# Kernel tuning notes

Hardware: AMD Instinct MI355X
Metric: run time of the kernel (lower is better)

Reference implementation:

```python
import jax, jax.numpy as jnp
import numpy as np

B, NPG, K_DYN, H, C = 8, 4096, 8, 2, 64   # graphs, nodes/graph, kNN, heads, head dim
N = B * NPG
E = 524288
CAP = 20.0
NEG = 0.2


def _leaky(x):
    return jax.nn.leaky_relu(x, NEG)


def _bn(x, g, b):
    # BatchNorm1d, training-mode statistics over the node dim (biased var, eps=1e-5)
    m = jnp.mean(x, 0)
    v = jnp.mean((x - m) ** 2, 0)
    return (x - m) * jax.lax.rsqrt(v + 1e-5) * g + b


def _gatv2(x, src, dst, wl, bl, wr, br, att, bias, ea=None, we=None):
    # PyG GATv2Conv, heads=H, concat=False (mean over heads), dropout in eval mode
    n = x.shape[0]
    xl = (x @ wl + bl).reshape(n, H, C)   # source transform
    xr = (x @ wr + br).reshape(n, H, C)   # target transform
    e = xl[src] + xr[dst]                 # [E,H,C]
    if ea is not None:
        e = e + (ea @ we).reshape(-1, H, C)
    e = _leaky(e)
    logit = jnp.sum(e * att, -1)          # [E,H]
    m = jax.ops.segment_max(logit, dst, num_segments=n)
    m = jnp.where(jnp.isfinite(m), m, 0.0)
    ex = jnp.exp(logit - m[dst])
    den = jax.ops.segment_sum(ex, dst, num_segments=n) + 1e-16
    alpha = ex / den[dst]                 # segment softmax over incoming edges
    out = jax.ops.segment_sum(alpha[..., None] * xl[src], dst, num_segments=n)
    return jnp.mean(out, 1) + bias        # concat=False -> mean over heads


def _dyn_agg(h, w1, b1, w2, b2):
    # dynamic kNN in feature space (per graph, detached), gather-MLP-mean aggregation
    h3 = h.reshape(B, NPG, -1)
    hd = jax.lax.stop_gradient(h3)
    sq = jnp.sum(hd * hd, -1)
    d = sq[:, :, None] + sq[:, None, :] - 2.0 * jnp.einsum('bnd,bmd->bnm', hd, hd)
    d = jnp.where(jnp.eye(NPG, dtype=bool), jnp.inf, d)  # exclude self
    _, idx = jax.lax.top_k(-d, K_DYN)                    # [B,n,K] nearest neighbors
    hn = jax.vmap(lambda hb, ib: hb[ib])(h3, idx)        # [B,n,K,D]
    hi = jnp.broadcast_to(h3[:, :, None, :], hn.shape)
    msg = jnp.concatenate([hi, hn - hi], -1)             # cat([h[row], h[col]-h[row]])
    msg = _leaky(msg @ w1 + b1) @ w2 + b2
    # every node emits exactly K edges -> scatter_add/count == mean over K
    return jnp.mean(msg, 2).reshape(N, -1)


def setup_inputs():
    key = jax.random.key(0)
    ks = iter(jax.random.split(key, 64))
    def rn(shape, scale=1.0):
        return jax.random.normal(next(ks), shape, dtype=jnp.float32) * scale
    hd = 64
    return {
        'x': rn((N, 5)),
        'edge_attr': rn((E, 6)),
        'edge_index': jax.random.randint(next(ks), (2, E), 0, N, dtype=jnp.int32),
        'g1_wl': rn((5, H * C), 0.3), 'g1_bl': rn((H * C,), 0.02),
        'g1_wr': rn((5, H * C), 0.3), 'g1_br': rn((H * C,), 0.02),
        'g1_we': rn((6, H * C), 0.3),
        'g1_att': rn((H, C), 0.1), 'g1_bias': rn((C,), 0.02),
        'bn1_g': jnp.ones((hd,), jnp.float32), 'bn1_b': jnp.zeros((hd,), jnp.float32),
        'em_w1': rn((2 * hd, hd), 0.08), 'em_b1': rn((hd,), 0.02),
        'em_w2': rn((hd, hd), 0.12), 'em_b2': rn((hd,), 0.02),
        'bn2_g': jnp.ones((hd,), jnp.float32), 'bn2_b': jnp.zeros((hd,), jnp.float32),
        'g2_wl': rn((hd, H * C), 0.12), 'g2_bl': rn((H * C,), 0.02),
        'g2_wr': rn((hd, H * C), 0.12), 'g2_br': rn((H * C,), 0.02),
        'g2_att': rn((H, C), 0.1), 'g2_bias': rn((C,), 0.02),
        'bn3_g': jnp.ones((hd,), jnp.float32), 'bn3_b': jnp.zeros((hd,), jnp.float32),
        'gate_w1': rn((hd, hd), 0.12), 'gate_b1': rn((hd,), 0.02),
        'gate_w2': rn((hd, 1), 0.12), 'gate_b2': rn((1,), 0.02),
        'ctx_w1': rn((hd, hd), 0.12), 'ctx_b1': rn((hd,), 0.02),
        'ctx_w2': rn((hd, hd), 0.12), 'ctx_b2': rn((hd,), 0.02),
        'dec_w1': rn((hd + hd + 5, 128), 0.09), 'dec_b1': rn((128,), 0.02),
        'ln_g': jnp.ones((128,), jnp.float32), 'ln_b': jnp.zeros((128,), jnp.float32),
        'dec_w2': rn((128, 64), 0.09), 'dec_b2': rn((64,), 0.02),
        'dec_w3': rn((64, 3), 0.12), 'dec_b3': rn((3,), 0.02),
    }


def reference(x, edge_attr, edge_index, g1_wl, g1_bl, g1_wr, g1_br, g1_we, g1_att, g1_bias,
              bn1_g, bn1_b, em_w1, em_b1, em_w2, em_b2, bn2_g, bn2_b,
              g2_wl, g2_bl, g2_wr, g2_br, g2_att, g2_bias, bn3_g, bn3_b,
              gate_w1, gate_b1, gate_w2, gate_b2, ctx_w1, ctx_b1, ctx_w2, ctx_b2,
              dec_w1, dec_b1, ln_g, ln_b, dec_w2, dec_b2, dec_w3, dec_b3):
    src, dst = edge_index[0], edge_index[1]
    h = _leaky(_bn(_gatv2(x, src, dst, g1_wl, g1_bl, g1_wr, g1_br, g1_att, g1_bias, edge_attr, g1_we), bn1_g, bn1_b))
    h = _leaky(_bn(_dyn_agg(h, em_w1, em_b1, em_w2, em_b2), bn2_g, bn2_b))
    h = _leaky(_bn(_gatv2(h, src, dst, g2_wl, g2_bl, g2_wr, g2_br, g2_att, g2_bias), bn3_g, bn3_b))
    # attentional pooling per graph (equal-sized graphs -> reshape instead of segment ops)
    h3 = h.reshape(B, NPG, -1)
    gate = jnp.tanh(h3 @ gate_w1 + gate_b1) @ gate_w2 + gate_b2   # [B,n,1]
    alpha = jax.nn.softmax(gate, axis=1)
    g = jnp.sum(alpha * h3, 1)                                    # [B,hd]
    g = _leaky(g @ ctx_w1 + ctx_b1) @ ctx_w2 + ctx_b2
    gfull = jnp.broadcast_to(g[:, None, :], (B, NPG, g.shape[-1])).reshape(N, -1)
    hf = jnp.concatenate([h, gfull, x], 1)                        # [N,133]
    d1 = _leaky(hf @ dec_w1 + dec_b1)
    mu = jnp.mean(d1, -1, keepdims=True)
    var = jnp.mean((d1 - mu) ** 2, -1, keepdims=True)
    d1 = (d1 - mu) * jax.lax.rsqrt(var + 1e-5) * ln_g + ln_b       # LayerNorm(128)
    d2 = _leaky(d1 @ dec_w2 + dec_b2)
    out3 = d2 @ dec_w3 + dec_b3
    return x[:, :3] + jnp.tanh(out3) * CAP
```

## Files before the change

kernel.cpp:

```cpp
#include <hip/hip_runtime.h>

#define NN   32768
#define NPG  4096
#define NGR  8
#define NE   524288
#define NEGS 0.2f

typedef float  v4f __attribute__((ext_vector_type(4)));
typedef short  v8s __attribute__((ext_vector_type(8)));

__device__ __forceinline__ float lrelu(float x){ return x > 0.f ? x : NEGS*x; }

__device__ __forceinline__ unsigned short f2bf(float v){
  unsigned int u = __float_as_uint(v);
  u = u + 0x7fffu + ((u >> 16) & 1u);
  return (unsigned short)(u >> 16);
}
__device__ __forceinline__ float bf2f(unsigned short s){
  return __uint_as_float(((unsigned int)s) << 16);
}

__global__ __launch_bounds__(256) void k_xform5(
    const float* __restrict__ x,
    const float* __restrict__ wl, const float* __restrict__ bl,
    const float* __restrict__ wr, const float* __restrict__ br,
    float* __restrict__ xl, float* __restrict__ xr) {
  int t = blockIdx.x * 256 + threadIdx.x;
  int n = t >> 7, oc = t & 127;
  const float* xp = x + n * 5;
  float a = bl[oc], b = br[oc];
  #pragma unroll
  for (int j = 0; j < 5; ++j) {
    float v = xp[j];
    a += v * wl[j * 128 + oc];
    b += v * wr[j * 128 + oc];
  }
  xl[t] = a; xr[t] = b;
}

__global__ __launch_bounds__(256) void k_count(const int* __restrict__ dst, int* __restrict__ cnt) {
  int e = blockIdx.x * 256 + threadIdx.x;
  atomicAdd(&cnt[dst[e]], 1);
}

__global__ __launch_bounds__(1024) void k_scan(const int* __restrict__ cnt,
                                               int* __restrict__ start, int* __restrict__ cur) {
  __shared__ int sh[1024];
  int t = threadIdx.x;
  int base = t * 32;
  int s = 0;
  for (int i = 0; i < 32; ++i) s += cnt[base + i];
  sh[t] = s;
  __syncthreads();
  for (int ofs = 1; ofs < 1024; ofs <<= 1) {
    int v = (t >= ofs) ? sh[t - ofs] : 0;
    __syncthreads();
    sh[t] += v;
    __syncthreads();
  }
  int run = sh[t] - s;
  for (int i = 0; i < 32; ++i) {
    start[base + i] = run; cur[base + i] = run;
    run += cnt[base + i];
  }
}

__global__ __launch_bounds__(256) void k_scatter(const int* __restrict__ dst,
                                                 const int* __restrict__ srcv,
                                                 int* __restrict__ cur,
                                                 int* __restrict__ bkt_e, int* __restrict__ bkt_s) {
  int e = blockIdx.x * 256 + threadIdx.x;
  int p = atomicAdd(&cur[dst[e]], 1);
  bkt_e[p] = e;
  bkt_s[p] = srcv[e];
}

template<int HAS_EA>
__global__ __launch_bounds__(256) void k_gat_edge(
    const float* __restrict__ xl, const float* __restrict__ xr,
    const float* __restrict__ ea,
    const float* __restrict__ we, const float* __restrict__ att,
    const float* __restrict__ bias,
    const int* __restrict__ start, const int* __restrict__ cnt,
    const int* __restrict__ bsrc, const int* __restrict__ bedge,
    float* __restrict__ out) {
  int wv = threadIdx.x >> 6, lane = threadIdx.x & 63;
  int n = blockIdx.x * 4 + wv;
  int s0 = start[n], deg = cnt[n];
  float xr0 = xr[n * 128 + lane], xr1 = xr[n * 128 + 64 + lane];
  float a0 = att[lane], a1 = att[64 + lane];
  float w0r[6], w1r[6];
  if (HAS_EA) {
    #pragma unroll
    for (int j = 0; j < 6; ++j) { w0r[j] = we[j * 128 + lane]; w1r[j] = we[j * 128 + 64 + lane]; }
  }
  float m0 = -1e30f, m1 = -1e30f, d0 = 0.f, d1 = 0.f, o0 = 0.f, o1 = 0.f;

  float l0 = 0.f, l1 = 0.f, ecur[6], enxt[6];
  int sNxt = 0;
  if (deg > 0) {
    int sCur = bsrc[s0];
    l0 = xl[sCur * 128 + lane]; l1 = xl[sCur * 128 + 64 + lane];
    if (HAS_EA) {
      int e = bedge[s0];
      #pragma unroll
      for (int j = 0; j < 6; ++j) ecur[j] = ea[e * 6 + j];
    }
    if (deg > 1) sNxt = bsrc[s0 + 1];
  }

  for (int i = 0; i < deg; ++i) {
    float l0c = l0, l1c = l1;
    if (i + 1 < deg) {
      l0 = xl[sNxt * 128 + lane]; l1 = xl[sNxt * 128 + 64 + lane];
      if (HAS_EA) {
        int e = bedge[s0 + i + 1];
        #pragma unroll
        for (int j = 0; j < 6; ++j) enxt[j] = ea[e * 6 + j];
      }
    }
    int sNN = (i + 2 < deg) ? bsrc[s0 + i + 2] : 0;

    float e0 = l0c + xr0, e1 = l1c + xr1;
    if (HAS_EA) {
      float p0 = 0.f, p1 = 0.f;
      #pragma unroll
      for (int j = 0; j < 6; ++j) { p0 += ecur[j] * w0r[j]; p1 += ecur[j] * w1r[j]; }
      e0 += p0; e1 += p1;
      #pragma unroll
      for (int j = 0; j < 6; ++j) ecur[j] = enxt[j];
    }
    e0 = lrelu(e0); e1 = lrelu(e1);
    float t0 = e0 * a0, t1 = e1 * a1;
    #pragma unroll
    for (int d = 32; d > 0; d >>= 1) { t0 += __shfl_xor(t0, d, 64); t1 += __shfl_xor(t1, d, 64); }
    if (t0 > m0) { float r = __expf(m0 - t0); o0 *= r; d0 *= r; m0 = t0; }
    float p0e = __expf(t0 - m0); d0 += p0e; o0 += p0e * l0c;
    if (t1 > m1) { float r = __expf(m1 - t1); o1 *= r; d1 *= r; m1 = t1; }
    float p1e = __expf(t1 - m1); d1 += p1e; o1 += p1e * l1c;
    sNxt = sNN;
  }
  float r0 = o0 / (d0 + 1e-16f);
  float r1 = o1 / (d1 + 1e-16f);
  out[n * 64 + lane] = 0.5f * (r0 + r1) + bias[lane];
}

__global__ __launch_bounds__(256) void k_bn_reduce(const float* __restrict__ h, float* __restrict__ stat) {
  float s = 0.f, s2 = 0.f;
  for (int i = blockIdx.x * 256 + threadIdx.x; i < NN * 64; i += gridDim.x * 256) {
    float v = h[i]; s += v; s2 += v * v;
  }
  __shared__ float sh[512];
  sh[threadIdx.x] = s; sh[256 + threadIdx.x] = s2;
  __syncthreads();
  if (threadIdx.x < 64) {
    int c = threadIdx.x;
    float a = sh[c] + sh[c + 64] + sh[c + 128] + sh[c + 192];
    float b = sh[256 + c] + sh[256 + c + 64] + sh[256 + c + 128] + sh[256 + c + 192];
    atomicAdd(&stat[c], a);
    atomicAdd(&stat[64 + c], b);
  }
}

__global__ void k_bn_final(const float* __restrict__ stat, const float* __restrict__ g,
                           const float* __restrict__ b, float* __restrict__ AB) {
  int c = threadIdx.x;
  float mean = stat[c] * (1.f / NN);
  float var  = stat[64 + c] * (1.f / NN) - mean * mean;
  float rstd = rsqrtf(var + 1e-5f);
  float A = g[c] * rstd;
  AB[c] = A; AB[64 + c] = b[c] - mean * A;
}

__global__ __launch_bounds__(256) void k_bn_apply(float* __restrict__ h, const float* __restrict__ AB) {
  int i = blockIdx.x * 256 + threadIdx.x;
  int c = i & 63;
  h[i] = lrelu(h[i] * AB[c] + AB[64 + c]);
}

__global__ __launch_bounds__(256) void k_split_sq(const float* __restrict__ h,
    unsigned short* __restrict__ hi, unsigned short* __restrict__ lo, float* __restrict__ sq) {
  int wv = threadIdx.x >> 6, lane = threadIdx.x & 63;
  int n = blockIdx.x * 4 + wv;
  int b = n >> 12, npg = n & (NPG - 1);
  float v = h[n * 64 + lane];
  unsigned short hu = f2bf(v);
  float hf = bf2f(hu);
  int idx = ((b * 8 + (lane >> 3)) * NPG + npg) * 8 + (lane & 7);
  hi[idx] = hu;
  lo[idx] = f2bf(v - hf);
  float s = v * v;
  #pragma unroll
  for (int d = 32; d > 0; d >>= 1) s += __shfl_xor(s, d, 64);
  if (lane == 0) sq[n] = s;
}

__global__ __launch_bounds__(256) void k_gram_topk(
    const unsigned short* __restrict__ hbhi, const unsigned short* __restrict__ hblo,
    const float* __restrict__ sq, int* __restrict__ cand) {
  __shared__ alignas(16) unsigned short Ahi[8 * 64 * 8],  Alo[8 * 64 * 8];
  __shared__ alignas(16) unsigned short Bhi[8 * 128 * 8], Blo[8 * 128 * 8];
  __shared__ float sqc[128];

  int tid = threadIdx.x, wv = tid >> 6, lane = tid & 63;
  int b = blockIdx.x >> 6, rblk = blockIdx.x & 63;
  int gbase = b * NPG, rowbase = gbase + rblk * 64;
  int l15 = lane & 15, l4 = lane >> 4;

  for (int chn = tid; chn < 512; chn += 256) {
    int s = chn >> 6, row = chn & 63;
    int gi = ((b * 8 + s) * NPG + rblk * 64 + row) * 8;
    *(uint4*)&Ahi[chn * 8] = *(const uint4*)&hbhi[gi];
    *(uint4*)&Alo[chn * 8] = *(const uint4*)&hblo[gi];
  }
  uint4 ph[4], pl[4];
  float psq = 0.f;
  {
    #pragma unroll
    for (int r = 0; r < 4; ++r) {
      int chn = tid + r * 256, s = chn >> 7, node = chn & 127;
      int gi = ((b * 8 + s) * NPG + node) * 8;
      ph[r] = *(const uint4*)&hbhi[gi];
      pl[r] = *(const uint4*)&hblo[gi];
    }
    if (tid < 128) psq = sq[gbase + tid];
  }
  __syncthreads();

  int rloc = wv * 16 + l15;
  int rnode = rowbase + rloc;
  float sqr = sq[rnode];
  v8s ofh[2], ofl[2];
  #pragma unroll
  for (int ks = 0; ks < 2; ++ks) {
    int s = ks * 4 + l4;
    ofh[ks] = *(v8s*)&Ahi[(s * 64 + rloc) * 8];
    ofl[ks] = *(v8s*)&Alo[(s * 64 + rloc) * 8];
  }

  float td[10]; int ti[10];
  #pragma unroll
  for (int j = 0; j < 10; ++j) { td[j] = 1e30f; ti[j] = 0x7fffffff; }

  for (int it = 0; it < NPG / 128; ++it) {
    #pragma unroll
    for (int r = 0; r < 4; ++r) {
      int chn = tid + r * 256;
      *(uint4*)&Bhi[chn * 8] = ph[r];
      *(uint4*)&Blo[chn * 8] = pl[r];
    }
    if (tid < 128) sqc[tid] = psq;
    if (it + 1 < NPG / 128) {
      int cbl = (it + 1) * 128;
      #pragma unroll
      for (int r = 0; r < 4; ++r) {
        int chn = tid + r * 256, s = chn >> 7, node = chn & 127;
        int gi = ((b * 8 + s) * NPG + cbl + node) * 8;
        ph[r] = *(const uint4*)&hbhi[gi];
        pl[r] = *(const uint4*)&hblo[gi];
      }
      if (tid < 128) psq = sq[gbase + cbl + tid];
    }
    __syncthreads();

    int cb = gbase + it * 128;
    for (int cg = 0; cg < 8; ++cg) {
      v8s ch0 = *(v8s*)&Bhi[((0 + l4) * 128 + cg * 16 + l15) * 8];
      v8s ch1 = *(v8s*)&Bhi[((4 + l4) * 128 + cg * 16 + l15) * 8];
      v8s cl0 = *(v8s*)&Blo[((0 + l4) * 128 + cg * 16 + l15) * 8];
      v8s cl1 = *(v8s*)&Blo[((4 + l4) * 128 + cg * 16 + l15) * 8];
      v4f accA = {0.f, 0.f, 0.f, 0.f}, accB = {0.f, 0.f, 0.f, 0.f};
      accA = __builtin_amdgcn_mfma_f32_16x16x32_bf16(ch0, ofh[0], accA, 0, 0, 0);
      accB = __builtin_amdgcn_mfma_f32_16x16x32_bf16(ch0, ofl[0], accB, 0, 0, 0);
      accA = __builtin_amdgcn_mfma_f32_16x16x32_bf16(ch1, ofh[1], accA, 0, 0, 0);
      accB = __builtin_amdgcn_mfma_f32_16x16x32_bf16(ch1, ofl[1], accB, 0, 0, 0);
      accB = __builtin_amdgcn_mfma_f32_16x16x32_bf16(cl0, ofh[0], accB, 0, 0, 0);
      accB = __builtin_amdgcn_mfma_f32_16x16x32_bf16(cl1, ofh[1], accB, 0, 0, 0);
      int cba = cb + cg * 16 + l4 * 4;
      #pragma unroll
      for (int r = 0; r < 4; ++r) {
        int cnode = cba + r;
        float dist = sqr + sqc[cg * 16 + l4 * 4 + r] - 2.f * (accA[r] + accB[r]);
        if (cnode != rnode && dist < td[9]) {
          float cd = dist; int ci = cnode;
          #pragma unroll
          for (int u = 0; u < 10; ++u) {
            bool bt = cd < td[u];
            float nd = bt ? cd : td[u]; int nc = bt ? ci : ti[u];
            float od = bt ? td[u] : cd; int oc = bt ? ti[u] : ci;
            td[u] = nd; ti[u] = nc; cd = od; ci = oc;
          }
        }
      }
    }
    __syncthreads();
  }

  float* mbd = (float*)Bhi;
  int*   mbi = (int*)Blo;
  #pragma unroll
  for (int j = 0; j < 10; ++j) {
    mbd[(rloc * 4 + l4) * 10 + j] = td[j];
    mbi[(rloc * 4 + l4) * 10 + j] = ti[j];
  }
  __syncthreads();
  if (tid < 64) {
    float fd[12]; int fi[12];
    #pragma unroll
    for (int j = 0; j < 12; ++j) { fd[j] = 1e30f; fi[j] = 0x7fffffff; }
    #pragma unroll 1
    for (int u = 0; u < 40; ++u) {
      float cd = mbd[tid * 40 + u];
      int   ci = mbi[tid * 40 + u];
      if (cd < fd[11] || (cd == fd[11] && ci < fi[11])) {
        #pragma unroll
        for (int v = 0; v < 12; ++v) {
          bool better = (cd < fd[v]) || (cd == fd[v] && ci < fi[v]);
          if (better) { float tf = fd[v]; int tq = fi[v]; fd[v] = cd; fi[v] = ci; cd = tf; ci = tq; }
        }
      }
    }
    #pragma unroll
    for (int j = 0; j < 12; ++j) cand[(rowbase + tid) * 12 + j] = fi[j];
  }
}

__global__ __launch_bounds__(256) void k_refine(
    const float* __restrict__ h, const int* __restrict__ cand, int* __restrict__ knn) {
  int wv = threadIdx.x >> 6, lane = threadIdx.x & 63;
  int n = blockIdx.x * 4 + wv;
  float hn = h[n * 64 + lane];
  float td[8]; int ti[8];
  #pragma unroll
  for (int j = 0; j < 8; ++j) { td[j] = 1e30f; ti[j] = 0x7fffffff; }
  #pragma unroll 1
  for (int j = 0; j < 12; ++j) {
    int c = cand[n * 12 + j];
    float df = h[c * 64 + lane] - hn;
    float s = df * df;
    #pragma unroll
    for (int d = 32; d > 0; d >>= 1) s += __shfl_xor(s, d, 64);
    if (s < td[7] || (s == td[7] && c < ti[7])) {
      float cd = s; int ci = c;
      #pragma unroll
      for (int u = 0; u < 8; ++u) {
        bool better = (cd < td[u]) || (cd == td[u] && ci < ti[u]);
        if (better) { float tf = td[u]; int tq = ti[u]; td[u] = cd; ti[u] = ci; cd = tf; ci = tq; }
      }
    }
  }
  #pragma unroll
  for (int u = 0; u < 8; ++u) {
    if (lane == u) knn[n * 8 + u] = ti[u];
  }
}

__global__ __launch_bounds__(256) void k_dynmlp(
    const float* __restrict__ h, const int* __restrict__ knn,
    const float* __restrict__ w1, const float* __restrict__ b1,
    const float* __restrict__ w2, const float* __restrict__ b2,
    float* __restrict__ out) {
  __shared__ alignas(16) float smem[128 * 64];
  __shared__ float outacc[8 * 64];
  int t = threadIdx.x;
  int nb = blockIdx.x * 8;
  for (int u = t; u < 512; u += 256) outacc[u] = 0.f;

  int p = t & 63;
  int n = nb + (p >> 3);
  int m = knn[n * 8 + (p & 7)];
  for (int qq = (t >> 6); qq < 32; qq += 4) {
    int j0 = qq * 4;
    float4 v;
    if (j0 < 64) {
      v = *(const float4*)(h + n * 64 + j0);
    } else {
      float4 a = *(const float4*)(h + m * 64 + (j0 - 64));
      float4 c = *(const float4*)(h + n * 64 + (j0 - 64));
      v.x = a.x - c.x; v.y = a.y - c.y; v.z = a.z - c.z; v.w = a.w - c.w;
    }
    smem[(j0 + 0) * 64 + p] = v.x;
    smem[(j0 + 1) * 64 + p] = v.y;
    smem[(j0 + 2) * 64 + p] = v.z;
    smem[(j0 + 3) * 64 + p] = v.w;
  }
  __syncthreads();

  int pq = t >> 4, cq = t & 15;
  float acc[4][4];
  #pragma unroll
  for (int c = 0; c < 4; ++c) {
    float bv = b1[cq * 4 + c];
    #pragma unroll
    for (int i = 0; i < 4; ++i) acc[i][c] = bv;
  }
  for (int j = 0; j < 128; ++j) {
    float4 av = *(float4*)&smem[j * 64 + pq * 4];
    float4 wv = *(const float4*)&w1[j * 64 + cq * 4];
    float aa[4] = {av.x, av.y, av.z, av.w};
    float ww[4] = {wv.x, wv.y, wv.z, wv.w};
    #pragma unroll
    for (int i = 0; i < 4; ++i)
      #pragma unroll
      for (int c = 0; c < 4; ++c) acc[i][c] += aa[i] * ww[c];
  }
  __syncthreads();
  #pragma unroll
  for (int c = 0; c < 4; ++c)
    #pragma unroll
    for (int i = 0; i < 4; ++i)
      smem[(cq * 4 + c) * 68 + pq * 4 + i] = lrelu(acc[i][c]);
  __syncthreads();

  float a2[4][4];
  #pragma unroll
  for (int i = 0; i < 4; ++i)
    #pragma unroll
    for (int c = 0; c < 4; ++c) a2[i][c] = 0.f;
  for (int j = 0; j < 64; ++j) {
    float4 av = *(float4*)&smem[j * 68 + pq * 4];
    float4 wv = *(const float4*)&w2[j * 64 + cq * 4];
    float aa[4] = {av.x, av.y, av.z, av.w};
    float ww[4] = {wv.x, wv.y, wv.z, wv.w};
    #pragma unroll
    for (int i = 0; i < 4; ++i)
      #pragma unroll
      for (int c = 0; c < 4; ++c) a2[i][c] += aa[i] * ww[c];
  }
  #pragma unroll
  for (int i = 0; i < 4; ++i) {
    int nloc = (pq * 4 + i) >> 3;
    #pragma unroll
    for (int c = 0; c < 4; ++c) atomicAdd(&outacc[nloc * 64 + cq * 4 + c], a2[i][c]);
  }
  __syncthreads();
  for (int u = t; u < 512; u += 256) {
    out[(nb + (u >> 6)) * 64 + (u & 63)] = outacc[u] * 0.125f + b2[u & 63];
  }
}

__global__ __launch_bounds__(256) void k_xform64(
    const float* __restrict__ h,
    const float* __restrict__ wl, const float* __restrict__ bl,
    const float* __restrict__ wr, const float* __restrict__ br,
    float* __restrict__ xl, float* __restrict__ xr) {
  __shared__ alignas(16) float hT[64 * 20];
  int t = threadIdx.x;
  int nb = blockIdx.x * 16;
  {
    int n = t >> 4, qj = t & 15;
    float4 v = *(const float4*)(h + (nb + n) * 64 + qj * 4);
    hT[(qj * 4 + 0) * 20 + n] = v.x;
    hT[(qj * 4 + 1) * 20 + n] = v.y;
    hT[(qj * 4 + 2) * 20 + n] = v.z;
    hT[(qj * 4 + 3) * 20 + n] = v.w;
  }
  __syncthreads();
  int pq = t >> 6, cq = t & 63;
  int oc = cq * 4;
  const float* wb; const float* bb; float* ob; int ocl;
  if (oc < 128) { wb = wl + oc;         bb = bl + oc;         ob = xl; ocl = oc; }
  else          { wb = wr + (oc - 128); bb = br + (oc - 128); ob = xr; ocl = oc - 128; }
  float acc[4][4];
  #pragma unroll
  for (int c = 0; c < 4; ++c) {
    float bv = bb[c];
    #pragma unroll
    for (int i = 0; i < 4; ++i) acc[i][c] = bv;
  }
  for (int j = 0; j < 64; ++j) {
    float4 av = *(float4*)&hT[j * 20 + pq * 4];
    float4 wv = *(const float4*)(wb + j * 128);
    float aa[4] = {av.x, av.y, av.z, av.w};
    float ww[4] = {wv.x, wv.y, wv.z, wv.w};
    #pragma unroll
    for (int i = 0; i < 4; ++i)
      #pragma unroll
      for (int c = 0; c < 4; ++c) acc[i][c] += aa[i] * ww[c];
  }
  #pragma unroll
  for (int i = 0; i < 4; ++i) {
    int n = nb + pq * 4 + i;
    #pragma unroll
    for (int c = 0; c < 4; ++c) ob[n * 128 + ocl + c] = acc[i][c];
  }
}

__global__ __launch_bounds__(256) void k_gate(
    const float* __restrict__ h3, const float* __restrict__ w1, const float* __restrict__ b1,
    const float* __restrict__ w2, const float* __restrict__ b2, float* __restrict__ gates) {
  __shared__ float hsh[4][64];
  int wv = threadIdx.x >> 6, lane = threadIdx.x & 63;
  int n = blockIdx.x * 4 + wv;
  hsh[wv][lane] = h3[n * 64 + lane];
  __syncthreads();
  float s = b1[lane];
  for (int j = 0; j < 64; ++j) s += hsh[wv][j] * w1[j * 64 + lane];
  float tv = tanhf(s) * w2[lane];
  #pragma unroll
  for (int d = 32; d > 0; d >>= 1) tv += __shfl_xor(tv, d, 64);
  if (lane == 0) gates[n] = tv + b2[0];
}

__global__ __launch_bounds__(1024) void k_pool(
    const float* __restrict__ gates, const float* __restrict__ h3,
    float* __restrict__ pexp, float* __restrict__ gpool) {
  int b = blockIdx.x, t = threadIdx.x;
  const float* g = gates + b * NPG;
  __shared__ float red[1024];
  float m = -1e30f;
  for (int i = t; i < NPG; i += 1024) m = fmaxf(m, g[i]);
  red[t] = m; __syncthreads();
  for (int s = 512; s > 0; s >>= 1) { if (t < s) red[t] = fmaxf(red[t], red[t + s]); __syncthreads(); }
  m = red[0]; __syncthreads();
  float sum = 0.f;
  for (int i = t; i < NPG; i += 1024) { float p = __expf(g[i] - m); pexp[b * NPG + i] = p; sum += p; }
  red[t] = sum; __syncthreads();
  for (int s = 512; s > 0; s >>= 1) { if (t < s) red[t] += red[t + s]; __syncthreads(); }
  float den = red[0];
  __syncthreads();
  int grp = t >> 6, c = t & 63;
  float acc = 0.f;
  for (int i = grp; i < NPG; i += 16) acc += pexp[b * NPG + i] * h3[(b * NPG + i) * 64 + c];
  red[t] = acc; __syncthreads();
  if (t < 64) {
    float a = 0.f;
    for (int qq = 0; qq < 16; ++qq) a += red[qq * 64 + t];
    gpool[b * 64 + t] = a / den;
  }
}

__global__ void k_ctx(const float* __restrict__ gpool,
                      const float* __restrict__ w1, const float* __restrict__ b1,
                      const float* __restrict__ w2, const float* __restrict__ b2,
                      float* __restrict__ gctx) {
  __shared__ float gsh[64], tsh[64];
  int b = blockIdx.x, c = threadIdx.x;
  gsh[c] = gpool[b * 64 + c];
  __syncthreads();
  float s = b1[c];
  for (int j = 0; j < 64; ++j) s += gsh[j] * w1[j * 64 + c];
  tsh[c] = lrelu(s);
  __syncthreads();
  float o = b2[c];
  for (int j = 0; j < 64; ++j) o += tsh[j] * w2[j * 64 + c];
  gctx[b * 64 + c] = o;
}

__global__ __launch_bounds__(128) void k_decoder(
    const float* __restrict__ h3, const float* __restrict__ gctx, const float* __restrict__ x,
    const float* __restrict__ w1, const float* __restrict__ b1,
    const float* __restrict__ lng, const float* __restrict__ lnb,
    const float* __restrict__ w2, const float* __restrict__ b2,
    const float* __restrict__ w3, const float* __restrict__ b3,
    float* __restrict__ out) {
  __shared__ alignas(16) float hf[16 * 136];
  __shared__ alignas(16) float dT[16 * 132];
  __shared__ float d2[16 * 65];
  __shared__ float mu[16], rs[16];
  int t = threadIdx.x;
  int nb = blockIdx.x * 16;
  int gb = nb >> 12;
  for (int u = t; u < 16 * 64; u += 128) { int p = u >> 6, j = u & 63; hf[p * 136 + j] = h3[(nb + p) * 64 + j]; }
  for (int u = t; u < 16 * 64; u += 128) { int p = u >> 6, j = u & 63; hf[p * 136 + 64 + j] = gctx[gb * 64 + j]; }
  for (int u = t; u < 16 * 5; u += 128) { int p = u / 5, j = u % 5; hf[p * 136 + 128 + j] = x[(nb + p) * 5 + j]; }
  __syncthreads();
  float acc[16];
  #pragma unroll
  for (int p = 0; p < 16; ++p) acc[p] = b1[t];
  for (int j4 = 0; j4 < 128; j4 += 4) {
    float w0 = w1[(j4 + 0) * 128 + t], wv1 = w1[(j4 + 1) * 128 + t];
    float wv2 = w1[(j4 + 2) * 128 + t], wv3 = w1[(j4 + 3) * 128 + t];
    #pragma unroll
    for (int p = 0; p < 16; ++p) {
      float4 hv = *(float4*)&hf[p * 136 + j4];
      acc[p] += hv.x * w0 + hv.y * wv1 + hv.z * wv2 + hv.w * wv3;
    }
  }
  for (int j = 128; j < 133; ++j) {
    float w = w1[j * 128 + t];
    #pragma unroll
    for (int p = 0; p < 16; ++p) acc[p] += hf[p * 136 + j] * w;
  }
  #pragma unroll
  for (int p = 0; p < 16; ++p) dT[p * 132 + t] = lrelu(acc[p]);
  __syncthreads();
  if (t < 16) {
    float s = 0.f, s2 = 0.f;
    for (int j = 0; j < 128; ++j) { float v = dT[t * 132 + j]; s += v; s2 += v * v; }
    float mn = s * (1.f / 128.f);
    float vr = s2 * (1.f / 128.f) - mn * mn;
    mu[t] = mn; rs[t] = rsqrtf(vr + 1e-5f);
  }
  __syncthreads();
  float lg = lng[t], lb = lnb[t];
  #pragma unroll
  for (int p = 0; p < 16; ++p) dT[p * 132 + t] = (dT[p * 132 + t] - mu[p]) * rs[p] * lg + lb;
  __syncthreads();
  if (t < 64) {
    float a2[16];
    #pragma unroll
    for (int p = 0; p < 16; ++p) a2[p] = b2[t];
    for (int j4 = 0; j4 < 128; j4 += 4) {
      float w0 = w2[(j4 + 0) * 64 + t], wv1 = w2[(j4 + 1) * 64 + t];
      float wv2 = w2[(j4 + 2) * 64 + t], wv3 = w2[(j4 + 3) * 64 + t];
      #pragma unroll
      for (int p = 0; p < 16; ++p) {
        float4 dv = *(float4*)&dT[p * 132 + j4];
        a2[p] += dv.x * w0 + dv.y * wv1 + dv.z * wv2 + dv.w * wv3;
      }
    }
    #pragma unroll
    for (int p = 0; p < 16; ++p) d2[p * 65 + t] = lrelu(a2[p]);
  }
  __syncthreads();
  if (t < 48) {
    int p = t / 3, k = t % 3;
    float o = b3[k];
    for (int j = 0; j < 64; ++j) o += d2[p * 65 + j] * w3[j * 3 + k];
    out[(nb + p) * 3 + k] = x[(nb + p) * 5 + k] + tanhf(o) * 20.0f;
  }
}

#define O_XL     0ul
#define O_HBHI   0ul
#define O_HBLO   4194304ul
#define O_SQ     8388608ul
#define O_KNN    8519680ul
#define O_XR     16777216ul
#define O_CAND   16777216ul
#define O_H1     33554432ul
#define O_H2     41943040ul
#define O_CNT    50331648ul
#define O_START  50462720ul
#define O_CUR    50593792ul
#define O_BKT    50724864ul
#define O_BSRC   52822016ul
#define O_STAT   54919168ul
#define O_AB     54919680ul
#define O_GATES  54920192ul
#define O_PEXP   55051264ul
#define O_GPOOL  55182336ul
#define O_GCTX   55184384ul

extern "C" void kernel_launch(void* const* d_in, const int* in_sizes, int n_in,
                              void* d_out, int out_size, void* d_ws, size_t ws_size,
                              hipStream_t stream) {
  (void)in_sizes; (void)n_in; (void)out_size; (void)ws_size;
  const float* x      = (const float*)d_in[0];
  const float* eattr  = (const float*)d_in[1];
  const int*   ei     = (const int*)d_in[2];
  const float* g1_wl  = (const float*)d_in[3];
  const float* g1_bl  = (const float*)d_in[4];
  const float* g1_wr  = (const float*)d_in[5];
  const float* g1_br  = (const float*)d_in[6];
  const float* g1_we  = (const float*)d_in[7];
  const float* g1_att = (const float*)d_in[8];
  const float* g1_bias= (const float*)d_in[9];
  const float* bn1_g  = (const float*)d_in[10];
  const float* bn1_b  = (const float*)d_in[11];
  const float* em_w1  = (const float*)d_in[12];
  const float* em_b1  = (const float*)d_in[13];
  const float* em_w2  = (const float*)d_in[14];
  const float* em_b2  = (const float*)d_in[15];
  const float* bn2_g  = (const float*)d_in[16];
  const float* bn2_b  = (const float*)d_in[17];
  const float* g2_wl  = (const float*)d_in[18];
  const float* g2_bl  = (const float*)d_in[19];
  const float* g2_wr  = (const float*)d_in[20];
  const float* g2_br  = (const float*)d_in[21];
  const float* g2_att = (const float*)d_in[22];
  const float* g2_bias= (const float*)d_in[23];
  const float* bn3_g  = (const float*)d_in[24];
  const float* bn3_b  = (const float*)d_in[25];
  const float* gt_w1  = (const float*)d_in[26];
  const float* gt_b1  = (const float*)d_in[27];
  const float* gt_w2  = (const float*)d_in[28];
  const float* gt_b2  = (const float*)d_in[29];
  const float* cx_w1  = (const float*)d_in[30];
  const float* cx_b1  = (const float*)d_in[31];
  const float* cx_w2  = (const float*)d_in[32];
  const float* cx_b2  = (const float*)d_in[33];
  const float* dc_w1  = (const float*)d_in[34];
  const float* dc_b1  = (const float*)d_in[35];
  const float* ln_g   = (const float*)d_in[36];
  const float* ln_b   = (const float*)d_in[37];
  const float* dc_w2  = (const float*)d_in[38];
  const float* dc_b2  = (const float*)d_in[39];
  const float* dc_w3  = (const float*)d_in[40];
  const float* dc_b3  = (const float*)d_in[41];

  char* ws = (char*)d_ws;
  float* xl    = (float*)(ws + O_XL);
  float* xr    = (float*)(ws + O_XR);
  float* h1    = (float*)(ws + O_H1);
  float* h2    = (float*)(ws + O_H2);
  int*   cnt   = (int*)(ws + O_CNT);
  int*   start = (int*)(ws + O_START);
  int*   cur   = (int*)(ws + O_CUR);
  int*   bkt   = (int*)(ws + O_BKT);
  int*   bsrc  = (int*)(ws + O_BSRC);
  unsigned short* hbhi = (unsigned short*)(ws + O_HBHI);
  unsigned short* hblo = (unsigned short*)(ws + O_HBLO);
  float* sq    = (float*)(ws + O_SQ);
  int*   knn   = (int*)(ws + O_KNN);
  int*   cand  = (int*)(ws + O_CAND);
  float* stat  = (float*)(ws + O_STAT);
  float* AB    = (float*)(ws + O_AB);
  float* gates = (float*)(ws + O_GATES);
  float* pexp  = (float*)(ws + O_PEXP);
  float* gpool = (float*)(ws + O_GPOOL);
  float* gctx  = (float*)(ws + O_GCTX);

  const int* src = ei;
  const int* dst = ei + NE;

  hipMemsetAsync(cnt, 0, NN * 4, stream);
  k_xform5<<<NN * 128 / 256, 256, 0, stream>>>(x, g1_wl, g1_bl, g1_wr, g1_br, xl, xr);
  k_count<<<NE / 256, 256, 0, stream>>>(dst, cnt);
  k_scan<<<1, 1024, 0, stream>>>(cnt, start, cur);
  k_scatter<<<NE / 256, 256, 0, stream>>>(dst, src, cur, bkt, bsrc);
  k_gat_edge<1><<<NN / 4, 256, 0, stream>>>(xl, xr, eattr, g1_we, g1_att, g1_bias,
                                            start, cnt, bsrc, bkt, h1);
  hipMemsetAsync(stat, 0, 512, stream);
  k_bn_reduce<<<256, 256, 0, stream>>>(h1, stat);
  k_bn_final<<<1, 64, 0, stream>>>(stat, bn1_g, bn1_b, AB);
  k_bn_apply<<<NN * 64 / 256, 256, 0, stream>>>(h1, AB);

  k_split_sq<<<NN / 4, 256, 0, stream>>>(h1, hbhi, hblo, sq);
  k_gram_topk<<<NGR * (NPG / 64), 256, 0, stream>>>(hbhi, hblo, sq, cand);
  k_refine<<<NN / 4, 256, 0, stream>>>(h1, cand, knn);
  k_dynmlp<<<NN / 8, 256, 0, stream>>>(h1, knn, em_w1, em_b1, em_w2, em_b2, h2);
  hipMemsetAsync(stat, 0, 512, stream);
  k_bn_reduce<<<256, 256, 0, stream>>>(h2, stat);
  k_bn_final<<<1, 64, 0, stream>>>(stat, bn2_g, bn2_b, AB);
  k_bn_apply<<<NN * 64 / 256, 256, 0, stream>>>(h2, AB);

  k_xform64<<<NN / 16, 256, 0, stream>>>(h2, g2_wl, g2_bl, g2_wr, g2_br, xl, xr);
  k_gat_edge<0><<<NN / 4, 256, 0, stream>>>(xl, xr, nullptr, nullptr, g2_att, g2_bias,
                                            start, cnt, bsrc, bkt, h1);
  hipMemsetAsync(stat, 0, 512, stream);
  k_bn_reduce<<<256, 256, 0, stream>>>(h1, stat);
  k_bn_final<<<1, 64, 0, stream>>>(stat, bn3_g, bn3_b, AB);
  k_bn_apply<<<NN * 64 / 256, 256, 0, stream>>>(h1, AB);

  k_gate<<<NN / 4, 256, 0, stream>>>(h1, gt_w1, gt_b1, gt_w2, gt_b2, gates);
  k_pool<<<NGR, 1024, 0, stream>>>(gates, h1, pexp, gpool);
  k_ctx<<<NGR, 64, 0, stream>>>(gpool, cx_w1, cx_b1, cx_w2, cx_b2, gctx);

  k_decoder<<<NN / 16, 128, 0, stream>>>(h1, gctx, x, dc_w1, dc_b1, ln_g, ln_b,
                                         dc_w2, dc_b2, dc_w3, dc_b3, (float*)d_out);
}
```

Baseline: 1.238 ms.

## Split gram-topk rows across more blocks and simplify candidate distance filtering

```diff
diff --git a/kernel.cpp b/kernel.cpp
--- a/kernel.cpp
+++ b/kernel.cpp
@@ -198,44 +198,42 @@
 __global__ __launch_bounds__(256) void k_gram_topk(
     const unsigned short* __restrict__ hbhi, const unsigned short* __restrict__ hblo,
     const float* __restrict__ sq, int* __restrict__ cand) {
-  __shared__ alignas(16) unsigned short Ahi[8 * 64 * 8],  Alo[8 * 64 * 8];
+  __shared__ alignas(16) unsigned short Ahi[8 * 32 * 8],  Alo[8 * 32 * 8];
   __shared__ alignas(16) unsigned short Bhi[8 * 128 * 8], Blo[8 * 128 * 8];
-  __shared__ float sqc[128];
+  __shared__ float sqch[128];
 
   int tid = threadIdx.x, wv = tid >> 6, lane = tid & 63;
-  int b = blockIdx.x >> 6, rblk = blockIdx.x & 63;
-  int gbase = b * NPG, rowbase = gbase + rblk * 64;
+  int b = blockIdx.x >> 7, rblk = blockIdx.x & 127;
+  int gbase = b * NPG, rowbase = gbase + rblk * 32;
   int l15 = lane & 15, l4 = lane >> 4;
-
-  for (int chn = tid; chn < 512; chn += 256) {
-    int s = chn >> 6, row = chn & 63;
-    int gi = ((b * 8 + s) * NPG + rblk * 64 + row) * 8;
-    *(uint4*)&Ahi[chn * 8] = *(const uint4*)&hbhi[gi];
-    *(uint4*)&Alo[chn * 8] = *(const uint4*)&hblo[gi];
+  int rg = wv >> 1, chalf = wv & 1;
+
+  {
+    int s = tid >> 5, row = tid & 31;
+    int gi = ((b * 8 + s) * NPG + rblk * 32 + row) * 8;
+    *(uint4*)&Ahi[tid * 8] = *(const uint4*)&hbhi[gi];
+    *(uint4*)&Alo[tid * 8] = *(const uint4*)&hblo[gi];
   }
   uint4 ph[4], pl[4];
   float psq = 0.f;
-  {
-    #pragma unroll
-    for (int r = 0; r < 4; ++r) {
-      int chn = tid + r * 256, s = chn >> 7, node = chn & 127;
-      int gi = ((b * 8 + s) * NPG + node) * 8;
-      ph[r] = *(const uint4*)&hbhi[gi];
-      pl[r] = *(const uint4*)&hblo[gi];
-    }
-    if (tid < 128) psq = sq[gbase + tid];
-  }
-  __syncthreads();
-
-  int rloc = wv * 16 + l15;
+  #pragma unroll
+  for (int r = 0; r < 4; ++r) {
+    int chn = tid + r * 256, s = chn >> 7, node = chn & 127;
+    int gi = ((b * 8 + s) * NPG + node) * 8;
+    ph[r] = *(const uint4*)&hbhi[gi];
+    pl[r] = *(const uint4*)&hblo[gi];
+  }
+  if (tid < 128) psq = 0.5f * sq[gbase + tid];
+  __syncthreads();
+
+  int rloc = rg * 16 + l15;
   int rnode = rowbase + rloc;
-  float sqr = sq[rnode];
   v8s ofh[2], ofl[2];
   #pragma unroll
   for (int ks = 0; ks < 2; ++ks) {
     int s = ks * 4 + l4;
-    ofh[ks] = *(v8s*)&Ahi[(s * 64 + rloc) * 8];
-    ofl[ks] = *(v8s*)&Alo[(s * 64 + rloc) * 8];
+    ofh[ks] = *(v8s*)&Ahi[(s * 32 + rloc) * 8];
+    ofl[ks] = *(v8s*)&Alo[(s * 32 + rloc) * 8];
   }
 
   float td[10]; int ti[10];
@@ -249,7 +247,7 @@
       *(uint4*)&Bhi[chn * 8] = ph[r];
       *(uint4*)&Blo[chn * 8] = pl[r];
     }
-    if (tid < 128) sqc[tid] = psq;
+    if (tid < 128) sqch[tid] = psq;
     if (it + 1 < NPG / 128) {
       int cbl = (it + 1) * 128;
       #pragma unroll
@@ -259,12 +257,14 @@
         ph[r] = *(const uint4*)&hbhi[gi];
         pl[r] = *(const uint4*)&hblo[gi];
       }
-      if (tid < 128) psq = sq[gbase + cbl + tid];
+      if (tid < 128) psq = 0.5f * sq[gbase + cbl + tid];
     }
     __syncthreads();
 
     int cb = gbase + it * 128;
-    for (int cg = 0; cg < 8; ++cg) {
+    #pragma unroll
+    for (int cc = 0; cc < 4; ++cc) {
+      int cg = chalf * 4 + cc;
       v8s ch0 = *(v8s*)&Bhi[((0 + l4) * 128 + cg * 16 + l15) * 8];
       v8s ch1 = *(v8s*)&Bhi[((4 + l4) * 128 + cg * 16 + l15) * 8];
       v8s cl0 = *(v8s*)&Blo[((0 + l4) * 128 + cg * 16 + l15) * 8];
@@ -276,19 +276,25 @@
       accB = __builtin_amdgcn_mfma_f32_16x16x32_bf16(ch1, ofl[1], accB, 0, 0, 0);
       accB = __builtin_amdgcn_mfma_f32_16x16x32_bf16(cl0, ofh[0], accB, 0, 0, 0);
       accB = __builtin_amdgcn_mfma_f32_16x16x32_bf16(cl1, ofh[1], accB, 0, 0, 0);
-      int cba = cb + cg * 16 + l4 * 4;
-      #pragma unroll
-      for (int r = 0; r < 4; ++r) {
-        int cnode = cba + r;
-        float dist = sqr + sqc[cg * 16 + l4 * 4 + r] - 2.f * (accA[r] + accB[r]);
-        if (cnode != rnode && dist < td[9]) {
-          float cd = dist; int ci = cnode;
-          #pragma unroll
-          for (int u = 0; u < 10; ++u) {
-            bool bt = cd < td[u];
-            float nd = bt ? cd : td[u]; int nc = bt ? ci : ti[u];
-            float od = bt ? td[u] : cd; int oc = bt ? ti[u] : ci;
-            td[u] = nd; ti[u] = nc; cd = od; ci = oc;
+      int kb = cg * 16 + l4 * 4;
+      float k0 = sqch[kb + 0] - (accA[0] + accB[0]);
+      float k1 = sqch[kb + 1] - (accA[1] + accB[1]);
+      float k2 = sqch[kb + 2] - (accA[2] + accB[2]);
+      float k3 = sqch[kb + 3] - (accA[3] + accB[3]);
+      float gmin = fminf(fminf(k0, k1), fminf(k2, k3));
+      if (gmin < td[9]) {
+        float kk[4] = {k0, k1, k2, k3};
+        #pragma unroll
+        for (int r = 0; r < 4; ++r) {
+          if (kk[r] < td[9]) {
+            float cd = kk[r]; int ci = cb + kb + r;
+            #pragma unroll
+            for (int u = 0; u < 10; ++u) {
+              bool bt = cd < td[u];
+              float nd = bt ? cd : td[u]; int nc = bt ? ci : ti[u];
+              float od = bt ? td[u] : cd; int oc = bt ? ti[u] : ci;
+              td[u] = nd; ti[u] = nc; cd = od; ci = oc;
+            }
           }
         }
       }
@@ -298,21 +304,23 @@
 
   float* mbd = (float*)Bhi;
   int*   mbi = (int*)Blo;
+  int listid = chalf * 4 + l4;
   #pragma unroll
   for (int j = 0; j < 10; ++j) {
-    mbd[(rloc * 4 + l4) * 10 + j] = td[j];
-    mbi[(rloc * 4 + l4) * 10 + j] = ti[j];
-  }
-  __syncthreads();
-  if (tid < 64) {
+    mbd[(rloc * 8 + listid) * 10 + j] = td[j];
+    mbi[(rloc * 8 + listid) * 10 + j] = ti[j];
+  }
+  __syncthreads();
+  if (tid < 32) {
+    int rn = rowbase + tid;
     float fd[12]; int fi[12];
     #pragma unroll
     for (int j = 0; j < 12; ++j) { fd[j] = 1e30f; fi[j] = 0x7fffffff; }
     #pragma unroll 1
-    for (int u = 0; u < 40; ++u) {
-      float cd = mbd[tid * 40 + u];
-      int   ci = mbi[tid * 40 + u];
-      if (cd < fd[11] || (cd == fd[11] && ci < fi[11])) {
+    for (int u = 0; u < 80; ++u) {
+      float cd = mbd[tid * 80 + u];
+      int   ci = mbi[tid * 80 + u];
+      if (ci != rn && (cd < fd[11] || (cd == fd[11] && ci < fi[11]))) {
         #pragma unroll
         for (int v = 0; v < 12; ++v) {
           bool better = (cd < fd[v]) || (cd == fd[v] && ci < fi[v]);
@@ -321,7 +329,7 @@
       }
     }
     #pragma unroll
-    for (int j = 0; j < 12; ++j) cand[(rowbase + tid) * 12 + j] = fi[j];
+    for (int j = 0; j < 12; ++j) cand[rn * 12 + j] = fi[j];
   }
 }
 
@@ -728,7 +736,7 @@
   k_bn_apply<<<NN * 64 / 256, 256, 0, stream>>>(h1, AB);
 
   k_split_sq<<<NN / 4, 256, 0, stream>>>(h1, hbhi, hblo, sq);
-  k_gram_topk<<<NGR * (NPG / 64), 256, 0, stream>>>(hbhi, hblo, sq, cand);
+  k_gram_topk<<<NGR * (NPG / 32), 256, 0, stream>>>(hbhi, hblo, sq, cand);
   k_refine<<<NN / 4, 256, 0, stream>>>(h1, cand, knn);
   k_dynmlp<<<NN / 8, 256, 0, stream>>>(h1, knn, em_w1, em_b1, em_w2, em_b2, h2);
   hipMemsetAsync(stat, 0, 512, stream);
```

Result: slower. 1.383 ms (+11.7%).

## Double-buffer kNN gram tiles and simplify distance key in gram_topk

Applied to the files above, without the earlier changes.

```diff
diff --git a/kernel.cpp b/kernel.cpp
--- a/kernel.cpp
+++ b/kernel.cpp
@@ -198,38 +198,37 @@
 __global__ __launch_bounds__(256) void k_gram_topk(
     const unsigned short* __restrict__ hbhi, const unsigned short* __restrict__ hblo,
     const float* __restrict__ sq, int* __restrict__ cand) {
-  __shared__ alignas(16) unsigned short Ahi[8 * 64 * 8],  Alo[8 * 64 * 8];
-  __shared__ alignas(16) unsigned short Bhi[8 * 128 * 8], Blo[8 * 128 * 8];
-  __shared__ float sqc[128];
+  __shared__ alignas(16) unsigned short Ahi[8 * 64 * 8], Alo[8 * 64 * 8];
+  __shared__ alignas(16) unsigned short Bhi[2 * 8 * 64 * 8];
+  __shared__ alignas(16) unsigned short Blo[2 * 8 * 64 * 8];
+  __shared__ float sqch[2][64];
 
   int tid = threadIdx.x, wv = tid >> 6, lane = tid & 63;
-  int b = blockIdx.x >> 6, rblk = blockIdx.x & 63;
+  int b = blockIdx.x & 7, rblk = blockIdx.x >> 3;
   int gbase = b * NPG, rowbase = gbase + rblk * 64;
   int l15 = lane & 15, l4 = lane >> 4;
 
-  for (int chn = tid; chn < 512; chn += 256) {
+  #pragma unroll
+  for (int r = 0; r < 2; ++r) {
+    int chn = tid + r * 256;
     int s = chn >> 6, row = chn & 63;
     int gi = ((b * 8 + s) * NPG + rblk * 64 + row) * 8;
     *(uint4*)&Ahi[chn * 8] = *(const uint4*)&hbhi[gi];
     *(uint4*)&Alo[chn * 8] = *(const uint4*)&hblo[gi];
   }
-  uint4 ph[4], pl[4];
-  float psq = 0.f;
-  {
-    #pragma unroll
-    for (int r = 0; r < 4; ++r) {
-      int chn = tid + r * 256, s = chn >> 7, node = chn & 127;
-      int gi = ((b * 8 + s) * NPG + node) * 8;
-      ph[r] = *(const uint4*)&hbhi[gi];
-      pl[r] = *(const uint4*)&hblo[gi];
-    }
-    if (tid < 128) psq = sq[gbase + tid];
-  }
+  #pragma unroll
+  for (int r = 0; r < 2; ++r) {
+    int chn = tid + r * 256;
+    int s = chn >> 6, node = chn & 63;
+    int gi = ((b * 8 + s) * NPG + node) * 8;
+    *(uint4*)&Bhi[chn * 8] = *(const uint4*)&hbhi[gi];
+    *(uint4*)&Blo[chn * 8] = *(const uint4*)&hblo[gi];
+  }
+  if (tid < 64) sqch[0][tid] = 0.5f * sq[gbase + tid];
   __syncthreads();
 
   int rloc = wv * 16 + l15;
   int rnode = rowbase + rloc;
-  float sqr = sq[rnode];
   v8s ofh[2], ofl[2];
   #pragma unroll
   for (int ks = 0; ks < 2; ++ks) {
@@ -242,33 +241,32 @@
   #pragma unroll
   for (int j = 0; j < 10; ++j) { td[j] = 1e30f; ti[j] = 0x7fffffff; }
 
-  for (int it = 0; it < NPG / 128; ++it) {
-    #pragma unroll
-    for (int r = 0; r < 4; ++r) {
-      int chn = tid + r * 256;
-      *(uint4*)&Bhi[chn * 8] = ph[r];
-      *(uint4*)&Blo[chn * 8] = pl[r];
-    }
-    if (tid < 128) sqc[tid] = psq;
-    if (it + 1 < NPG / 128) {
-      int cbl = (it + 1) * 128;
-      #pragma unroll
-      for (int r = 0; r < 4; ++r) {
-        int chn = tid + r * 256, s = chn >> 7, node = chn & 127;
-        int gi = ((b * 8 + s) * NPG + cbl + node) * 8;
-        ph[r] = *(const uint4*)&hbhi[gi];
-        pl[r] = *(const uint4*)&hblo[gi];
-      }
-      if (tid < 128) psq = sq[gbase + cbl + tid];
-    }
-    __syncthreads();
-
-    int cb = gbase + it * 128;
-    for (int cg = 0; cg < 8; ++cg) {
-      v8s ch0 = *(v8s*)&Bhi[((0 + l4) * 128 + cg * 16 + l15) * 8];
-      v8s ch1 = *(v8s*)&Bhi[((4 + l4) * 128 + cg * 16 + l15) * 8];
-      v8s cl0 = *(v8s*)&Blo[((0 + l4) * 128 + cg * 16 + l15) * 8];
-      v8s cl1 = *(v8s*)&Blo[((4 + l4) * 128 + cg * 16 + l15) * 8];
+  int cur = 0;
+  for (int it = 0; it < NPG / 64; ++it) {
+    bool more = (it + 1 < NPG / 64);
+    uint4 nh0, nh1, nl0, nl1;
+    float nsq = 0.f;
+    if (more) {
+      int tb = (it + 1) * 64;
+      int s0 = tid >> 6, n0 = tid & 63;
+      int chn1 = tid + 256, s1 = chn1 >> 6, n1 = chn1 & 63;
+      int g0 = ((b * 8 + s0) * NPG + tb + n0) * 8;
+      int g1 = ((b * 8 + s1) * NPG + tb + n1) * 8;
+      nh0 = *(const uint4*)&hbhi[g0];
+      nh1 = *(const uint4*)&hbhi[g1];
+      nl0 = *(const uint4*)&hblo[g0];
+      nl1 = *(const uint4*)&hblo[g1];
+      if (tid < 64) nsq = 0.5f * sq[gbase + tb + tid];
+    }
+
+    int base = cur * 512;
+    int cb = gbase + it * 64;
+    #pragma unroll
+    for (int cg = 0; cg < 4; ++cg) {
+      v8s ch0 = *(v8s*)&Bhi[(base + (0 + l4) * 64 + cg * 16 + l15) * 8];
+      v8s ch1 = *(v8s*)&Bhi[(base + (4 + l4) * 64 + cg * 16 + l15) * 8];
+      v8s cl0 = *(v8s*)&Blo[(base + (0 + l4) * 64 + cg * 16 + l15) * 8];
+      v8s cl1 = *(v8s*)&Blo[(base + (4 + l4) * 64 + cg * 16 + l15) * 8];
       v4f accA = {0.f, 0.f, 0.f, 0.f}, accB = {0.f, 0.f, 0.f, 0.f};
       accA = __builtin_amdgcn_mfma_f32_16x16x32_bf16(ch0, ofh[0], accA, 0, 0, 0);
       accB = __builtin_amdgcn_mfma_f32_16x16x32_bf16(ch0, ofl[0], accB, 0, 0, 0);
@@ -276,24 +274,40 @@
       accB = __builtin_amdgcn_mfma_f32_16x16x32_bf16(ch1, ofl[1], accB, 0, 0, 0);
       accB = __builtin_amdgcn_mfma_f32_16x16x32_bf16(cl0, ofh[0], accB, 0, 0, 0);
       accB = __builtin_amdgcn_mfma_f32_16x16x32_bf16(cl1, ofh[1], accB, 0, 0, 0);
-      int cba = cb + cg * 16 + l4 * 4;
-      #pragma unroll
-      for (int r = 0; r < 4; ++r) {
-        int cnode = cba + r;
-        float dist = sqr + sqc[cg * 16 + l4 * 4 + r] - 2.f * (accA[r] + accB[r]);
-        if (cnode != rnode && dist < td[9]) {
-          float cd = dist; int ci = cnode;
-          #pragma unroll
-          for (int u = 0; u < 10; ++u) {
-            bool bt = cd < td[u];
-            float nd = bt ? cd : td[u]; int nc = bt ? ci : ti[u];
-            float od = bt ? td[u] : cd; int oc = bt ? ti[u] : ci;
-            td[u] = nd; ti[u] = nc; cd = od; ci = oc;
+      int kb = cg * 16 + l4 * 4;
+      float k0 = sqch[cur][kb + 0] - (accA[0] + accB[0]);
+      float k1 = sqch[cur][kb + 1] - (accA[1] + accB[1]);
+      float k2 = sqch[cur][kb + 2] - (accA[2] + accB[2]);
+      float k3 = sqch[cur][kb + 3] - (accA[3] + accB[3]);
+      float gmin = fminf(fminf(k0, k1), fminf(k2, k3));
+      if (gmin < td[9]) {
+        float kk[4] = {k0, k1, k2, k3};
+        #pragma unroll
+        for (int r = 0; r < 4; ++r) {
+          if (kk[r] < td[9]) {
+            float cd = kk[r]; int ci = cb + kb + r;
+            #pragma unroll
+            for (int u = 0; u < 10; ++u) {
+              bool bt = cd < td[u];
+              float nd = bt ? cd : td[u]; int nc = bt ? ci : ti[u];
+              float od = bt ? td[u] : cd; int oc = bt ? ti[u] : ci;
+              td[u] = nd; ti[u] = nc; cd = od; ci = oc;
+            }
           }
         }
       }
     }
+
+    if (more) {
+      int nb_ = (cur ^ 1) * 4096;
+      *(uint4*)&Bhi[nb_ + tid * 8]         = nh0;
+      *(uint4*)&Bhi[nb_ + (tid + 256) * 8] = nh1;
+      *(uint4*)&Blo[nb_ + tid * 8]         = nl0;
+      *(uint4*)&Blo[nb_ + (tid + 256) * 8] = nl1;
+      if (tid < 64) sqch[cur ^ 1][tid] = nsq;
+    }
     __syncthreads();
+    cur ^= 1;
   }
 
   float* mbd = (float*)Bhi;
@@ -305,6 +319,7 @@
   }
   __syncthreads();
   if (tid < 64) {
+    int rn = rowbase + tid;
     float fd[12]; int fi[12];
     #pragma unroll
     for (int j = 0; j < 12; ++j) { fd[j] = 1e30f; fi[j] = 0x7fffffff; }
@@ -312,7 +327,7 @@
     for (int u = 0; u < 40; ++u) {
       float cd = mbd[tid * 40 + u];
       int   ci = mbi[tid * 40 + u];
-      if (cd < fd[11] || (cd == fd[11] && ci < fi[11])) {
+      if (ci != rn && (cd < fd[11] || (cd == fd[11] && ci < fi[11]))) {
         #pragma unroll
         for (int v = 0; v < 12; ++v) {
           bool better = (cd < fd[v]) || (cd == fd[v] && ci < fi[v]);
@@ -321,7 +336,7 @@
       }
     }
     #pragma unroll
-    for (int j = 0; j < 12; ++j) cand[(rowbase + tid) * 12 + j] = fi[j];
+    for (int j = 0; j < 12; ++j) cand[rn * 12 + j] = fi[j];
   }
 }
 
```

New measurement: 1.160 ms. 1.07x faster.
